# Optimization experiments

Hardware: AMD Instinct MI355X
Metric: run time of the kernel (lower is better)

Reference implementation:

```python
import math
import jax, jax.numpy as jnp
import numpy as np

DIM = 192
HEADS = 6
WIN = (16, 16)
N = WIN[0] * WIN[1]
B_ = 256
NW = 64
CPB_HIDDEN = 512


def _relative_coords_table(window_size):
    Wh, Ww = window_size
    h = np.arange(-(Wh - 1), Wh, dtype=np.float32)
    w = np.arange(-(Ww - 1), Ww, dtype=np.float32)
    table = np.stack(np.meshgrid(h, w, indexing='ij'), axis=-1)[None]  # (1, 2Wh-1, 2Ww-1, 2)
    table[..., 0] /= (Wh - 1)
    table[..., 1] /= (Ww - 1)
    table *= 8.0
    table = np.sign(table) * np.log2(np.abs(table) + 1.0) / np.log2(8.0)
    return table.astype(np.float32)


def _relative_position_index(window_size):
    Wh, Ww = window_size
    coords = np.stack(np.meshgrid(np.arange(Wh), np.arange(Ww), indexing='ij'))  # (2, Wh, Ww)
    flat = coords.reshape(2, -1)
    rel = flat[:, :, None] - flat[:, None, :]  # (2, N, N)
    rel = rel.transpose(1, 2, 0).astype(np.int64)
    rel[..., 0] += Wh - 1
    rel[..., 1] += Ww - 1
    rel[..., 0] *= 2 * Ww - 1
    return rel.sum(-1)  # (N, N)


def setup_inputs() -> dict:
    key = jax.random.key(0)
    ks = jax.random.split(key, 9)
    s = 1.0 / math.sqrt(DIM)
    inp = {
        'x': jax.random.normal(ks[0], (B_, N, DIM), dtype=jnp.float32),
        'mask': jax.random.normal(ks[1], (NW, N, N), dtype=jnp.float32),
        'qkv_w': jax.random.normal(ks[2], (3 * DIM, DIM), dtype=jnp.float32) * s,
        'qkv_b': jnp.zeros((3 * DIM,), dtype=jnp.float32),
        'proj_w': jax.random.normal(ks[3], (DIM, DIM), dtype=jnp.float32) * s,
        'proj_b': jnp.zeros((DIM,), dtype=jnp.float32),
        'logit_scale': jnp.full((HEADS, 1, 1), math.log(10.0), dtype=jnp.float32),
        'cpb_w1': jax.random.normal(ks[4], (CPB_HIDDEN, 2), dtype=jnp.float32) * (1.0 / math.sqrt(2.0)),
        'cpb_b1': jnp.zeros((CPB_HIDDEN,), dtype=jnp.float32),
        'cpb_w2': jax.random.normal(ks[5], (HEADS, CPB_HIDDEN), dtype=jnp.float32) * (1.0 / math.sqrt(CPB_HIDDEN)),
        'coords_table': jnp.asarray(_relative_coords_table(WIN)),
        'rel_index': jnp.asarray(_relative_position_index(WIN)),
    }
    return inp


def reference(x, mask, qkv_w, qkv_b, proj_w, proj_b, logit_scale,
              cpb_w1, cpb_b1, cpb_w2, coords_table, rel_index):
    Bw, n, C = x.shape
    H = logit_scale.shape[0]
    Dh = C // H
    eps = 1e-12

    qkv = x @ qkv_w.T + qkv_b                             # (B_, N, 3C)
    qkv = qkv.reshape(Bw, n, 3, H, Dh).transpose(2, 0, 3, 1, 4)
    q, k, v = qkv[0], qkv[1], qkv[2]                      # (B_, H, N, Dh)

    qn = q / jnp.maximum(jnp.linalg.norm(q, axis=-1, keepdims=True), eps)
    kn = k / jnp.maximum(jnp.linalg.norm(k, axis=-1, keepdims=True), eps)
    attn = jnp.einsum('bhnd,bhmd->bhnm', qn, kn)

    scale = jnp.exp(jnp.minimum(logit_scale, math.log(1.0 / 0.01)))  # (H,1,1)
    attn = attn * scale[None]

    # CPB MLP bias: (1, 2Wh-1, 2Ww-1, 2) -> (-1, H), gather, sigmoid-scale
    hbt = jax.nn.relu(coords_table @ cpb_w1.T + cpb_b1) @ cpb_w2.T   # (1, 2Wh-1, 2Ww-1, H)
    bias_table = hbt.reshape(-1, H)
    bias = bias_table[rel_index.reshape(-1)].reshape(n, n, H).transpose(2, 0, 1)
    attn = attn + 16.0 * jax.nn.sigmoid(bias)[None]

    nW = mask.shape[0]
    attn = attn.reshape(Bw // nW, nW, H, n, n) + mask[None, :, None]
    attn = attn.reshape(Bw, H, n, n)

    attn = jax.nn.softmax(attn, axis=-1)
    out = jnp.einsum('bhnm,bhmd->bhnd', attn, v)
    out = out.transpose(0, 2, 1, 3).reshape(Bw, n, C)
    return out @ proj_w.T + proj_b
```

## Files before the change

### kernel.cpp

```cpp
#include <hip/hip_runtime.h>

using bf16 = __bf16;
typedef bf16 bf16x4 __attribute__((ext_vector_type(4)));
typedef bf16 bf16x8 __attribute__((ext_vector_type(8)));
typedef float f32x4 __attribute__((ext_vector_type(4)));

__device__ __forceinline__ int swz192(int row, int col) {
  return row * 192 + (col ^ ((row & 7) << 3));
}
__device__ __forceinline__ int qk_idx(int row, int col) {
  return (row >> 1) * 64 + (row & 1) * 32 + (col ^ (((row >> 1) & 3) << 3));
}
__device__ __forceinline__ int vt_idx(int d, int n) {
  return d * 256 + (((n + ((d >> 3) << 4)) & 255) ^ ((d & 7) << 3));
}
__device__ __forceinline__ int p_idx4(int wv, int r, int c) {
  return wv * 1024 + r * 64 + (c ^ ((r & 7) << 3));
}

#define LOG2E 1.44269504088896f
#define GLOAD_LDS(src, dst)                                                     \
  __builtin_amdgcn_global_load_lds(                                             \
      (const __attribute__((address_space(1))) void*)(src),                     \
      (__attribute__((address_space(3))) void*)(dst), 16, 0, 0)

__global__ __launch_bounds__(256) void k_qkv(const bf16* __restrict__ A,
                                             const bf16* __restrict__ W,
                                             const float* __restrict__ bias,
                                             const float* __restrict__ lsc,
                                             bf16* __restrict__ Op,
                                             const float* __restrict__ bt,
                                             const int* __restrict__ rel,
                                             float* __restrict__ biasfT) {
  __shared__ bf16 As[64 * 192];
  __shared__ bf16 Bs[64 * 192];
  const int bid = blockIdx.x;
  const int t = threadIdx.x;

  if (bid >= 9216) {
    const int idx = (bid - 9216) * 256 + t;
    const int hh = idx >> 16;
    const int jj = (idx >> 8) & 255;
    const int i = idx & 255;
    const float v = bt[rel[i * 256 + jj] * 6 + hh];
    biasfT[idx] = LOG2E * 16.f / (1.f + __builtin_amdgcn_exp2f(-LOG2E * v));
    return;
  }

  const int xcd = bid & 7;
  const int j = bid >> 3;
  const int m0 = (xcd + 8 * (j / 9)) * 64;
  const int n0 = (j % 9) * 64;

#pragma unroll
  for (int i = 0; i < 6; ++i) {
    const int f = t + i * 256;
    const int row = f / 24, c8 = f % 24;
    const int csw = (c8 ^ (row & 7)) * 8;
    GLOAD_LDS(&A[(m0 + row) * 192 + csw], &As[f * 8]);
    GLOAD_LDS(&W[(n0 + row) * 192 + csw], &Bs[f * 8]);
  }
  __syncthreads();

  const int w = t >> 6, lane = t & 63, lo = lane & 15, hi = lane >> 4;
  const int wm = (w >> 1) * 32, wn = (w & 1) * 32;
  f32x4 acc[2][2];
#pragma unroll
  for (int a = 0; a < 2; ++a)
#pragma unroll
    for (int c = 0; c < 2; ++c) acc[a][c] = f32x4{0.f, 0.f, 0.f, 0.f};

#pragma unroll
  for (int ks = 0; ks < 6; ++ks) {
    const int k0 = ks * 32 + hi * 8;
    bf16x8 af[2], bfr[2];
#pragma unroll
    for (int ri = 0; ri < 2; ++ri)
      af[ri] = *reinterpret_cast<const bf16x8*>(&As[swz192(wm + ri * 16 + lo, k0)]);
#pragma unroll
    for (int ci = 0; ci < 2; ++ci)
      bfr[ci] = *reinterpret_cast<const bf16x8*>(&Bs[swz192(wn + ci * 16 + lo, k0)]);
#pragma unroll
    for (int ri = 0; ri < 2; ++ri)
#pragma unroll
      for (int ci = 0; ci < 2; ++ci)
        acc[ri][ci] = __builtin_amdgcn_mfma_f32_16x16x32_bf16(af[ri], bfr[ci], acc[ri][ci], 0, 0, 0);
  }

  const int cb = n0 + wn;
  const bool donorm = (cb < 384);
  float smul = 1.f;
  if (cb < 192)
    smul = expf(fminf(lsc[cb >> 5], 4.605170185988091f)) * LOG2E;
  const int col0 = cb + lo;
  const float b0 = bias[col0], b1 = bias[col0 + 16];
#pragma unroll
  for (int ri = 0; ri < 2; ++ri)
#pragma unroll
    for (int rr = 0; rr < 4; ++rr) {
      float v0 = acc[ri][0][rr] + b0;
      float v1 = acc[ri][1][rr] + b1;
      if (donorm) {
        float ss = v0 * v0 + v1 * v1;
        ss += __shfl_xor(ss, 1, 16);
        ss += __shfl_xor(ss, 2, 16);
        ss += __shfl_xor(ss, 4, 16);
        ss += __shfl_xor(ss, 8, 16);
        const float rn = smul / fmaxf(sqrtf(ss), 1e-12f);
        v0 *= rn;
        v1 *= rn;
      }
      const int row = m0 + wm + ri * 16 + hi * 4 + rr;
      Op[row * 576 + col0] = (bf16)v0;
      Op[row * 576 + col0 + 16] = (bf16)v1;
    }
}

template <int NT>
__global__ __launch_bounds__(256) void k_gemm(const bf16* __restrict__ A,
                                              const bf16* __restrict__ W,
                                              const float* __restrict__ bias,
                                              float* __restrict__ Op, int Ntot) {
  __shared__ bf16 As[64 * 192];
  __shared__ bf16 Bs[64 * 192];
  const int bid = blockIdx.x;
  const int xcd = bid & 7;
  const int j = bid >> 3;
  const int m0 = (xcd + 8 * (j / NT)) * 64;
  const int n0 = (j % NT) * 64;
  const int t = threadIdx.x;

#pragma unroll
  for (int i = 0; i < 6; ++i) {
    const int f = t + i * 256;
    const int row = f / 24, c8 = f % 24;
    const int csw = (c8 ^ (row & 7)) * 8;
    GLOAD_LDS(&A[(m0 + row) * 192 + csw], &As[f * 8]);
    GLOAD_LDS(&W[(n0 + row) * 192 + csw], &Bs[f * 8]);
  }
  __syncthreads();

  const int w = t >> 6, lane = t & 63, lo = lane & 15, hi = lane >> 4;
  const int wm = (w >> 1) * 32, wn = (w & 1) * 32;
  f32x4 acc[2][2];
#pragma unroll
  for (int a = 0; a < 2; ++a)
#pragma unroll
    for (int c = 0; c < 2; ++c) acc[a][c] = f32x4{0.f, 0.f, 0.f, 0.f};

#pragma unroll
  for (int ks = 0; ks < 6; ++ks) {
    const int k0 = ks * 32 + hi * 8;
    bf16x8 af[2], bfr[2];
#pragma unroll
    for (int ri = 0; ri < 2; ++ri)
      af[ri] = *reinterpret_cast<const bf16x8*>(&As[swz192(wm + ri * 16 + lo, k0)]);
#pragma unroll
    for (int ci = 0; ci < 2; ++ci)
      bfr[ci] = *reinterpret_cast<const bf16x8*>(&Bs[swz192(wn + ci * 16 + lo, k0)]);
#pragma unroll
    for (int ri = 0; ri < 2; ++ri)
#pragma unroll
      for (int ci = 0; ci < 2; ++ci)
        acc[ri][ci] = __builtin_amdgcn_mfma_f32_16x16x32_bf16(af[ri], bfr[ci], acc[ri][ci], 0, 0, 0);
  }

#pragma unroll
  for (int ri = 0; ri < 2; ++ri)
#pragma unroll
    for (int ci = 0; ci < 2; ++ci) {
      const int col = n0 + wn + ci * 16 + lo;
      const float bv = bias[col];
#pragma unroll
      for (int rr = 0; rr < 4; ++rr) {
        const int row = m0 + wm + ri * 16 + hi * 4 + rr;
        __builtin_nontemporal_store(acc[ri][ci][rr] + bv, &Op[row * Ntot + col]);
      }
    }
}

__global__ __launch_bounds__(256) void k_prep(
    const float* __restrict__ x, bf16* __restrict__ xb,
    const float* __restrict__ qkv_w, bf16* __restrict__ qkv_wb,
    const float* __restrict__ proj_w, bf16* __restrict__ proj_wb,
    const float* __restrict__ mask, bf16* __restrict__ maskT,
    const float* __restrict__ ct, const float* __restrict__ w1,
    const float* __restrict__ b1, const float* __restrict__ w2,
    float* __restrict__ bt) {
  __shared__ float tile[64][65];
  const int bid = blockIdx.x;
  if (bid < 6216) {
    const float* in;
    bf16* o;
    int vb;
    bool nt = false;
    if (bid < 6144) { in = x; o = xb; vb = bid; nt = true; }
    else if (bid < 6198) { in = qkv_w; o = qkv_wb; vb = bid - 6144; }
    else { in = proj_w; o = proj_wb; vb = bid - 6198; }
    const int i = (vb * 256 + threadIdx.x) * 8;
    f32x4 a, b;
    if (nt) {
      a = __builtin_nontemporal_load(reinterpret_cast<const f32x4*>(&in[i]));
      b = __builtin_nontemporal_load(reinterpret_cast<const f32x4*>(&in[i + 4]));
    } else {
      a = *reinterpret_cast<const f32x4*>(&in[i]);
      b = *reinterpret_cast<const f32x4*>(&in[i + 4]);
    }
    bf16x8 v;
    v[0] = (bf16)a[0]; v[1] = (bf16)a[1]; v[2] = (bf16)a[2]; v[3] = (bf16)a[3];
    v[4] = (bf16)b[0]; v[5] = (bf16)b[1]; v[6] = (bf16)b[2]; v[7] = (bf16)b[3];
    *reinterpret_cast<bf16x8*>(&o[i]) = v;
  } else if (bid < 7240) {
    const int rem = bid - 6216;
    const int mb = rem >> 4;
    const int it = (rem & 15) >> 2, jt = rem & 3;
    const int tx = threadIdx.x & 63, ty = threadIdx.x >> 6;
    const float* mp = mask + mb * 65536;
#pragma unroll
    for (int rr = 0; rr < 16; ++rr)
      tile[rr * 4 + ty][tx] = mp[(it * 64 + rr * 4 + ty) * 256 + jt * 64 + tx];
    __syncthreads();
    bf16* op = maskT + mb * 65536;
#pragma unroll
    for (int rr = 0; rr < 16; ++rr)
      op[(jt * 64 + rr * 4 + ty) * 256 + it * 64 + tx] = (bf16)(LOG2E * tile[tx][rr * 4 + ty]);
  } else {
    const int wid = (bid - 7240) * 4 + (threadIdx.x >> 6);
    if (wid < 5766) {
      const int r = wid / 6, hh = wid % 6;
      const int lane = threadIdx.x & 63;
      const float t0 = ct[r * 2], t1 = ct[r * 2 + 1];
      float acc = 0.f;
#pragma unroll
      for (int jj = 0; jj < 8; ++jj) {
        const int j = lane + jj * 64;
        float hv = fmaf(w1[j * 2], t0, fmaf(w1[j * 2 + 1], t1, b1[j]));
        hv = fmaxf(hv, 0.f);
        acc = fmaf(hv, w2[hh * 512 + j], acc);
      }
      acc += __shfl_xor(acc, 1);
      acc += __shfl_xor(acc, 2);
      acc += __shfl_xor(acc, 4);
      acc += __shfl_xor(acc, 8);
      acc += __shfl_xor(acc, 16);
      acc += __shfl_xor(acc, 32);
      if (lane == 0) bt[wid] = acc;
    }
  }
}

__global__ __launch_bounds__(256) void k_attn(const bf16* __restrict__ qkv,
                                              const bf16* __restrict__ maskT,
                                              const float* __restrict__ biasfT,
                                              bf16* __restrict__ aout) {
  __shared__ bf16 ksh[256 * 32];
  __shared__ bf16 vts[32 * 256];
  __shared__ bf16 ps[4 * 16 * 64];

  const int bid = blockIdx.x;
  const int x = bid & 7, i = bid >> 3;
  const int mb = x * 8 + i / 24;
  const int rem = i % 24;
  const int b = (rem / 6) * 64 + mb;
  const int h = rem % 6;
  const int t = threadIdx.x;

  const int rsub = t >> 2;
  const int c4s = t & 3;
#pragma unroll
  for (int p = 0; p < 4; ++p) {
    const int row = p * 64 + rsub;
    const int base = (b * 256 + row) * 576 + h * 32 + c4s * 8;
    *reinterpret_cast<bf16x8*>(&ksh[qk_idx(row, c4s * 8)]) =
        *reinterpret_cast<const bf16x8*>(&qkv[base + 192]);
    bf16x8 v = *reinterpret_cast<const bf16x8*>(&qkv[base + 384]);
#pragma unroll
    for (int jj = 0; jj < 8; ++jj) vts[vt_idx(c4s * 8 + jj, row)] = v[jj];
  }
  __syncthreads();

  const int w = t >> 6, lane = t & 63, lo = lane & 15, hi = lane >> 4;
  const float* bT = biasfT + (h << 16);
  const bf16* mT = maskT + (mb << 16);
  const bf16* qbase = qkv + (b * 256) * 576 + h * 32;

  bf16x8 afn = *reinterpret_cast<const bf16x8*>(&qbase[(w * 16 + lo) * 576 + hi * 8]);

  f32x4 bvp[4];
  bf16x4 mvp[4];
  {
    const int rbase0 = w * 16 + hi * 4;
#pragma unroll
    for (int c = 0; c < 4; ++c) {
      const int col = c * 16 + lo;
      bvp[c] = *reinterpret_cast<const f32x4*>(&bT[col * 256 + rbase0]);
      mvp[c] = *reinterpret_cast<const bf16x4*>(&mT[col * 256 + rbase0]);
    }
  }

  for (int rgi = 0; rgi < 4; ++rgi) {
    const int rg = rgi * 4 + w;
    const int rbase = rg * 16 + hi * 4;
    const bf16x8 af = afn;
    if (rgi < 3)
      afn = *reinterpret_cast<const bf16x8*>(&qbase[((rg + 4) * 16 + lo) * 576 + hi * 8]);

    f32x4 po0 = {0.f, 0.f, 0.f, 0.f}, po1 = {0.f, 0.f, 0.f, 0.f};
    float sum[4] = {0.f, 0.f, 0.f, 0.f};

#pragma unroll
    for (int ph = 0; ph < 4; ++ph) {
      f32x4 bv[4];
      bf16x4 mv[4];
#pragma unroll
      for (int c = 0; c < 4; ++c) { bv[c] = bvp[c]; mv[c] = mvp[c]; }
      if (ph < 3) {
#pragma unroll
        for (int c = 0; c < 4; ++c) {
          const int col = (ph + 1) * 64 + c * 16 + lo;
          bvp[c] = *reinterpret_cast<const f32x4*>(&bT[col * 256 + rbase]);
          mvp[c] = *reinterpret_cast<const bf16x4*>(&mT[col * 256 + rbase]);
        }
      } else if (rgi < 3) {
#pragma unroll
        for (int c = 0; c < 4; ++c) {
          const int col = c * 16 + lo;
          bvp[c] = *reinterpret_cast<const f32x4*>(&bT[col * 256 + rbase + 64]);
          mvp[c] = *reinterpret_cast<const bf16x4*>(&mT[col * 256 + rbase + 64]);
        }
      }
      bf16x8 kf[4];
#pragma unroll
      for (int c4i = 0; c4i < 4; ++c4i) {
        const int ct = ph * 4 + c4i;
        kf[c4i] = *reinterpret_cast<const bf16x8*>(&ksh[qk_idx(ct * 16 + lo, hi * 8)]);
      }
      f32x4 a[4];
#pragma unroll
      for (int c4i = 0; c4i < 4; ++c4i) {
        f32x4 z = {0.f, 0.f, 0.f, 0.f};
        a[c4i] = __builtin_amdgcn_mfma_f32_16x16x32_bf16(af, kf[c4i], z, 0, 0, 0);
      }
#pragma unroll
      for (int c4i = 0; c4i < 4; ++c4i)
#pragma unroll
        for (int rr = 0; rr < 4; ++rr) {
          const float s = a[c4i][rr] + bv[c4i][rr] + (float)mv[c4i][rr];
          const float p = __builtin_amdgcn_exp2f(s);
          sum[rr] += p;
          ps[p_idx4(w, hi * 4 + rr, c4i * 16 + lo)] = (bf16)p;
        }
#pragma unroll
      for (int kb = 0; kb < 2; ++kb) {
        const bf16x8 pa = *reinterpret_cast<const bf16x8*>(&ps[p_idx4(w, lo, kb * 32 + hi * 8)]);
        const bf16x8 b0 = *reinterpret_cast<const bf16x8*>(&vts[vt_idx(lo, ph * 64 + kb * 32 + hi * 8)]);
        const bf16x8 b1 = *reinterpret_cast<const bf16x8*>(&vts[vt_idx(16 + lo, ph * 64 + kb * 32 + hi * 8)]);
        po0 = __builtin_amdgcn_mfma_f32_16x16x32_bf16(pa, b0, po0, 0, 0, 0);
        po1 = __builtin_amdgcn_mfma_f32_16x16x32_bf16(pa, b1, po1, 0, 0, 0);
      }
    }
#pragma unroll
    for (int rr = 0; rr < 4; ++rr) {
      float s = sum[rr];
      s += __shfl_xor(s, 1, 16);
      s += __shfl_xor(s, 2, 16);
      s += __shfl_xor(s, 4, 16);
      s += __shfl_xor(s, 8, 16);
      sum[rr] = 1.f / s;
    }
#pragma unroll
    for (int rr = 0; rr < 4; ++rr) {
      const int ob = (b * 256 + rbase + rr) * 192 + h * 32;
      aout[ob + lo] = (bf16)(po0[rr] * sum[rr]);
      aout[ob + 16 + lo] = (bf16)(po1[rr] * sum[rr]);
    }
  }
}

extern "C" void kernel_launch(void* const* d_in, const int* in_sizes, int n_in,
                              void* d_out, int out_size, void* d_ws, size_t ws_size,
                              hipStream_t stream) {
  const float* x      = (const float*)d_in[0];
  const float* mask   = (const float*)d_in[1];
  const float* qkv_w  = (const float*)d_in[2];
  const float* qkv_b  = (const float*)d_in[3];
  const float* proj_w = (const float*)d_in[4];
  const float* proj_b = (const float*)d_in[5];
  const float* lsc    = (const float*)d_in[6];
  const float* cpb_w1 = (const float*)d_in[7];
  const float* cpb_b1 = (const float*)d_in[8];
  const float* cpb_w2 = (const float*)d_in[9];
  const float* ctab   = (const float*)d_in[10];
  const int*   relidx = (const int*)d_in[11];

  char* ws = (char*)d_ws;
  bf16*  qkvb   = (bf16*)(ws);
  bf16*  xb     = (bf16*)(ws + 75497472);
  bf16*  aoutb  = (bf16*)(ws + 75497472);
  float* biasfT = (float*)(ws + 100663296);
  bf16*  maskTb = (bf16*)(ws + 102236160);
  float* bt     = (float*)(ws + 110624768);
  bf16*  qkv_wb = (bf16*)(ws + 110647840);
  bf16*  proj_wb= (bf16*)(ws + 110869024);

  k_prep<<<8682, 256, 0, stream>>>(x, xb, qkv_w, qkv_wb, proj_w, proj_wb,
                                   mask, maskTb, ctab, cpb_w1, cpb_b1, cpb_w2, bt);
  k_qkv<<<10752, 256, 0, stream>>>(xb, qkv_wb, qkv_b, lsc, qkvb, bt, relidx, biasfT);
  k_attn<<<1536, 256, 0, stream>>>(qkvb, maskTb, biasfT, aoutb);
  k_gemm<3><<<3072, 256, 0, stream>>>(aoutb, proj_wb, proj_b, (float*)d_out, 192);
}
```

Measured before the change: 185.1 us.

## Fuse fp32-to-bf16 conversion of x into the QKV GEMM tile load

The separate prep pass that converted x to a bf16 workspace buffer is removed. The QKV GEMM now reads fp32 x directly with vector loads, converts it in registers, and writes swizzled bf16 into LDS. This drops one full write and re-read of the activation tensor. In exchange, each A tile is loaded as twice the bytes through registers instead of async global-to-LDS copies, and each tile is re-read by all nine column blocks, so more L2 traffic is possible.

```diff
diff --git a/kernel.cpp b/kernel.cpp
--- a/kernel.cpp
+++ b/kernel.cpp
@@ -24,7 +24,7 @@
       (const __attribute__((address_space(1))) void*)(src),                     \
       (__attribute__((address_space(3))) void*)(dst), 16, 0, 0)
 
-__global__ __launch_bounds__(256) void k_qkv(const bf16* __restrict__ A,
+__global__ __launch_bounds__(256) void k_qkv(const float* __restrict__ A,
                                              const bf16* __restrict__ W,
                                              const float* __restrict__ bias,
                                              const float* __restrict__ lsc,
@@ -57,8 +57,16 @@
     const int f = t + i * 256;
     const int row = f / 24, c8 = f % 24;
     const int csw = (c8 ^ (row & 7)) * 8;
-    GLOAD_LDS(&A[(m0 + row) * 192 + csw], &As[f * 8]);
     GLOAD_LDS(&W[(n0 + row) * 192 + csw], &Bs[f * 8]);
+  }
+#pragma unroll
+  for (int i = 0; i < 12; ++i) {
+    const int f = t + i * 256;
+    const int row = f / 48, c4 = f % 48;
+    const f32x4 v = *reinterpret_cast<const f32x4*>(&A[(m0 + row) * 192 + c4 * 4]);
+    bf16x4 hv;
+    hv[0] = (bf16)v[0]; hv[1] = (bf16)v[1]; hv[2] = (bf16)v[2]; hv[3] = (bf16)v[3];
+    *reinterpret_cast<bf16x4*>(&As[swz192(row, c4 * 4)]) = hv;
   }
   __syncthreads();
 
@@ -180,7 +188,6 @@
 }
 
 __global__ __launch_bounds__(256) void k_prep(
-    const float* __restrict__ x, bf16* __restrict__ xb,
     const float* __restrict__ qkv_w, bf16* __restrict__ qkv_wb,
     const float* __restrict__ proj_w, bf16* __restrict__ proj_wb,
     const float* __restrict__ mask, bf16* __restrict__ maskT,
@@ -189,29 +196,21 @@
     float* __restrict__ bt) {
   __shared__ float tile[64][65];
   const int bid = blockIdx.x;
-  if (bid < 6216) {
+  if (bid < 72) {
     const float* in;
     bf16* o;
     int vb;
-    bool nt = false;
-    if (bid < 6144) { in = x; o = xb; vb = bid; nt = true; }
-    else if (bid < 6198) { in = qkv_w; o = qkv_wb; vb = bid - 6144; }
-    else { in = proj_w; o = proj_wb; vb = bid - 6198; }
+    if (bid < 54) { in = qkv_w; o = qkv_wb; vb = bid; }
+    else { in = proj_w; o = proj_wb; vb = bid - 54; }
     const int i = (vb * 256 + threadIdx.x) * 8;
-    f32x4 a, b;
-    if (nt) {
-      a = __builtin_nontemporal_load(reinterpret_cast<const f32x4*>(&in[i]));
-      b = __builtin_nontemporal_load(reinterpret_cast<const f32x4*>(&in[i + 4]));
-    } else {
-      a = *reinterpret_cast<const f32x4*>(&in[i]);
-      b = *reinterpret_cast<const f32x4*>(&in[i + 4]);
-    }
+    const f32x4 a = *reinterpret_cast<const f32x4*>(&in[i]);
+    const f32x4 b = *reinterpret_cast<const f32x4*>(&in[i + 4]);
     bf16x8 v;
     v[0] = (bf16)a[0]; v[1] = (bf16)a[1]; v[2] = (bf16)a[2]; v[3] = (bf16)a[3];
     v[4] = (bf16)b[0]; v[5] = (bf16)b[1]; v[6] = (bf16)b[2]; v[7] = (bf16)b[3];
     *reinterpret_cast<bf16x8*>(&o[i]) = v;
-  } else if (bid < 7240) {
-    const int rem = bid - 6216;
+  } else if (bid < 1096) {
+    const int rem = bid - 72;
     const int mb = rem >> 4;
     const int it = (rem & 15) >> 2, jt = rem & 3;
     const int tx = threadIdx.x & 63, ty = threadIdx.x >> 6;
@@ -225,7 +224,7 @@
     for (int rr = 0; rr < 16; ++rr)
       op[(jt * 64 + rr * 4 + ty) * 256 + it * 64 + tx] = (bf16)(LOG2E * tile[tx][rr * 4 + ty]);
   } else {
-    const int wid = (bid - 7240) * 4 + (threadIdx.x >> 6);
+    const int wid = (bid - 1096) * 4 + (threadIdx.x >> 6);
     if (wid < 5766) {
       const int r = wid / 6, hh = wid % 6;
       const int lane = threadIdx.x & 63;
@@ -395,7 +394,6 @@
 
   char* ws = (char*)d_ws;
   bf16*  qkvb   = (bf16*)(ws);
-  bf16*  xb     = (bf16*)(ws + 75497472);
   bf16*  aoutb  = (bf16*)(ws + 75497472);
   float* biasfT = (float*)(ws + 100663296);
   bf16*  maskTb = (bf16*)(ws + 102236160);
@@ -403,9 +401,9 @@
   bf16*  qkv_wb = (bf16*)(ws + 110647840);
   bf16*  proj_wb= (bf16*)(ws + 110869024);
 
-  k_prep<<<8682, 256, 0, stream>>>(x, xb, qkv_w, qkv_wb, proj_w, proj_wb,
+  k_prep<<<2538, 256, 0, stream>>>(qkv_w, qkv_wb, proj_w, proj_wb,
                                    mask, maskTb, ctab, cpb_w1, cpb_b1, cpb_w2, bt);
-  k_qkv<<<10752, 256, 0, stream>>>(xb, qkv_wb, qkv_b, lsc, qkvb, bt, relidx, biasfT);
+  k_qkv<<<10752, 256, 0, stream>>>(x, qkv_wb, qkv_b, lsc, qkvb, bt, relidx, biasfT);
   k_attn<<<1536, 256, 0, stream>>>(qkvb, maskTb, biasfT, aoutb);
   k_gemm<3><<<3072, 256, 0, stream>>>(aoutb, proj_wb, proj_b, (float*)d_out, 192);
 }
```

Measured after the change: 182.7 us, median of 2. About the same (-1.3%).
